# Optimization experiments

Measured on AMD Instinct MI355X. Metric: run time of the kernel, lower is better.

Reference implementation:

```python
import jax, jax.numpy as jnp
import numpy as np

B, S, E, H = 2, 2048, 1024, 16
D = E // H  # head_dim = 64


def _rope(x):
    # x: (B, H, S, D); torchtune-style interleaved rotary embedding
    s, d = x.shape[-2], x.shape[-1]
    inv_freq = 1.0 / (10000.0 ** (jnp.arange(0, d, 2, dtype=jnp.float32) / d))  # (d/2,)
    freqs = jnp.arange(s, dtype=jnp.float32)[:, None] * inv_freq[None, :]       # (S, d/2)
    cos, sin = jnp.cos(freqs), jnp.sin(freqs)
    x1, x2 = x[..., 0::2], x[..., 1::2]
    o1 = x1 * cos - x2 * sin
    o2 = x2 * cos + x1 * sin
    return jnp.stack([o1, o2], axis=-1).reshape(x.shape)


def setup_inputs() -> dict:
    key = jax.random.key(0)
    kx, kq, kk, kv, ko = jax.random.split(key, 5)
    std = 1.0 / np.sqrt(E)
    return {
        "x": jax.random.normal(kx, (B, S, E), dtype=jnp.float32),
        "W_q": jax.random.normal(kq, (E, E), dtype=jnp.float32) * std,
        "W_k": jax.random.normal(kk, (E, E), dtype=jnp.float32) * std,
        "W_v": jax.random.normal(kv, (E, E), dtype=jnp.float32) * std,
        "W_o": jax.random.normal(ko, (E, E), dtype=jnp.float32) * std,
    }


def reference(x, W_q, W_k, W_v, W_o):
    b, s, e = x.shape
    h, d = H, e // H
    # nn.Linear: y = x @ W.T  (weights are (out, in))
    q = (x @ W_q.T).reshape(b, s, h, d).transpose(0, 2, 1, 3)  # (B,H,S,D)
    k = (x @ W_k.T).reshape(b, s, h, d).transpose(0, 2, 1, 3)
    v = (x @ W_v.T).reshape(b, s, h, d).transpose(0, 2, 1, 3)
    q = _rope(q)
    k = _rope(k)
    attn_scale = 1.0 / np.sqrt(e)  # NOTE: scales by sqrt(hidden_dim), as in source
    scores = jnp.einsum("bhsd,bhtd->bhst", q, k) * attn_scale  # (B,H,S,S)
    causal = jnp.triu(jnp.ones((s, s), dtype=bool), k=1)
    scores = jnp.where(causal, -jnp.inf, scores)
    probs = jax.nn.softmax(scores, axis=-1)  # dropout is identity in eval
    out = jnp.einsum("bhst,bhtd->bhsd", probs, v)
    out = out.transpose(0, 2, 1, 3).reshape(b, s, e)
    return out @ W_o.T
```

## Files before the change

### kernel.cpp

```cpp
#include <hip/hip_runtime.h>
#include <hip/hip_bf16.h>

#define BATCH 2
#define SEQ   2048
#define EMB   1024
#define NH    16
#define HD    64
#define MROWS (BATCH*SEQ)
#define NX    (MROWS*EMB)
#define NW    (EMB*EMB)

using f32x4  = __attribute__((ext_vector_type(4))) float;
using bf16x8 = __attribute__((ext_vector_type(8))) short;

#define GLOBAL_AS(p) ((const __attribute__((address_space(1))) void*)(p))
#define LDS_AS(p)    ((__attribute__((address_space(3))) void*)(p))

#define ROPE_L2 0.4152410118609203f
#define QSCALE  0.045084220027780106f

__global__ void fused_cast_kernel(const float* __restrict__ x,
                                  const float* __restrict__ Wq,
                                  const float* __restrict__ Wk,
                                  const float* __restrict__ Wv,
                                  const float* __restrict__ Wo,
                                  __hip_bfloat16* __restrict__ xb,
                                  __hip_bfloat16* __restrict__ Wqkvb,
                                  __hip_bfloat16* __restrict__ Wob) {
    size_t i8 = (size_t)(blockIdx.x * 256 + threadIdx.x) * 8;
    const float* src;
    __hip_bfloat16* dst;
    if (i8 < (size_t)NX) {
        src = x + i8;
        dst = xb + i8;
    } else {
        size_t w = i8 - NX;
        int which = (int)(w >> 20);
        size_t local = w & (NW - 1);
        if (which < 3) {
            src = (which == 0 ? Wq : (which == 1 ? Wk : Wv)) + local;
            dst = Wqkvb + w;
        } else {
            src = Wo + local;
            dst = Wob + local;
        }
    }
    float4 a = *(const float4*)(src);
    float4 b = *(const float4*)(src + 4);
    union { uint4 u; ushort s[8]; } o;
    const float* f = (const float*)&a;
#pragma unroll
    for (int j = 0; j < 4; ++j) {
        __hip_bfloat16 h = __float2bfloat16(f[j]);
        o.s[j] = *(ushort*)&h;
    }
    f = (const float*)&b;
#pragma unroll
    for (int j = 0; j < 4; ++j) {
        __hip_bfloat16 h = __float2bfloat16(f[j]);
        o.s[4 + j] = *(ushort*)&h;
    }
    *(uint4*)dst = o.u;
}

__global__ __launch_bounds__(256) void gemm_qkv_kernel(
        const __hip_bfloat16* __restrict__ A,
        const __hip_bfloat16* __restrict__ W,
        __hip_bfloat16* __restrict__ Qo,
        __hip_bfloat16* __restrict__ Ko,
        __hip_bfloat16* __restrict__ Vo, int M, int K) {
    __shared__ __hip_bfloat16 As[128 * 64];
    __shared__ __hip_bfloat16 Bs[128 * 64];

    const int tid  = threadIdx.x;
    const int wave = tid >> 6;
    const int lane = tid & 63;
    const int quad = lane >> 4;
    const int l16  = lane & 15;
    const int m0   = blockIdx.y * 128;
    const int n0   = blockIdx.x * 128;
    const int wm   = (wave >> 1) * 64;
    const int wn   = (wave & 1) * 64;

    f32x4 acc[4][4] = {};

    for (int k0 = 0; k0 < K; k0 += 64) {
#pragma unroll
        for (int it = 0; it < 4; ++it) {
            int flat = (wave * 4 + it) * 64 + lane;
            int row  = flat >> 3;
            int g    = flat & 7;
            const __hip_bfloat16* ga = A + (size_t)(m0 + row) * K + k0 + g * 8;
            const __hip_bfloat16* gb = W + (size_t)(n0 + row) * K + k0 + g * 8;
            __builtin_amdgcn_global_load_lds(GLOBAL_AS(ga),
                LDS_AS(As + (size_t)(wave * 4 + it) * 512), 16, 0, 0);
            __builtin_amdgcn_global_load_lds(GLOBAL_AS(gb),
                LDS_AS(Bs + (size_t)(wave * 4 + it) * 512), 16, 0, 0);
        }
        __syncthreads();

#pragma unroll
        for (int kk = 0; kk < 2; ++kk) {
            bf16x8 af[4], bfr[4];
#pragma unroll
            for (int i = 0; i < 4; ++i) {
                af[i]  = *(const bf16x8*)(&As[(wm + i * 16 + l16) * 64 + (kk * 4 + quad) * 8]);
                bfr[i] = *(const bf16x8*)(&Bs[(wn + i * 16 + l16) * 64 + (kk * 4 + quad) * 8]);
            }
#pragma unroll
            for (int i = 0; i < 4; ++i)
#pragma unroll
                for (int j = 0; j < 4; ++j)
                    acc[i][j] = __builtin_amdgcn_mfma_f32_16x16x32_bf16(
                        af[i], bfr[j], acc[i][j], 0, 0, 0);
        }
        __syncthreads();
    }

    const int tens = n0 >> 10;
    __hip_bfloat16* outp = (tens == 0) ? Qo : ((tens == 1) ? Ko : Vo);
    const int nbase = n0 & 1023;
#pragma unroll
    for (int i = 0; i < 4; ++i)
#pragma unroll
        for (int j = 0; j < 4; ++j) {
            int col  = nbase + wn + j * 16 + l16;
            int row0 = m0 + wm + i * 16 + quad * 4;
#pragma unroll
            for (int rr = 0; rr < 4; ++rr)
                outp[(size_t)(row0 + rr) * EMB + col] = __float2bfloat16(acc[i][j][rr]);
        }
}

__global__ __launch_bounds__(256) void gemm_oproj_kernel(
        const __hip_bfloat16* __restrict__ A,
        const __hip_bfloat16* __restrict__ Bm,
        float* __restrict__ C, int M, int N, int K) {
    __shared__ __hip_bfloat16 As[128 * 64];
    __shared__ __hip_bfloat16 Bs[64 * 64];

    const int tid  = threadIdx.x;
    const int wave = tid >> 6;
    const int lane = tid & 63;
    const int quad = lane >> 4;
    const int l16  = lane & 15;
    const int m0   = blockIdx.y * 128;
    const int n0   = blockIdx.x * 64;
    const int wm   = (wave >> 1) * 64;
    const int wn   = (wave & 1) * 32;

    f32x4 acc[4][2] = {};

    for (int k0 = 0; k0 < K; k0 += 64) {
#pragma unroll
        for (int it = 0; it < 4; ++it) {
            int flat = (wave * 4 + it) * 64 + lane;
            int row  = flat >> 3;
            int g    = flat & 7;
            const __hip_bfloat16* ga = A + (size_t)(m0 + row) * K + k0 + g * 8;
            __builtin_amdgcn_global_load_lds(GLOBAL_AS(ga),
                LDS_AS(As + (size_t)(wave * 4 + it) * 512), 16, 0, 0);
        }
#pragma unroll
        for (int it = 0; it < 2; ++it) {
            int flat = (wave * 2 + it) * 64 + lane;
            int row  = flat >> 3;
            int g    = flat & 7;
            const __hip_bfloat16* gb = Bm + (size_t)(n0 + row) * K + k0 + g * 8;
            __builtin_amdgcn_global_load_lds(GLOBAL_AS(gb),
                LDS_AS(Bs + (size_t)(wave * 2 + it) * 512), 16, 0, 0);
        }
        __syncthreads();

#pragma unroll
        for (int kk = 0; kk < 2; ++kk) {
            bf16x8 af[4], bfr[2];
#pragma unroll
            for (int i = 0; i < 4; ++i)
                af[i] = *(const bf16x8*)(&As[(wm + i * 16 + l16) * 64 + (kk * 4 + quad) * 8]);
#pragma unroll
            for (int j = 0; j < 2; ++j)
                bfr[j] = *(const bf16x8*)(&Bs[(wn + j * 16 + l16) * 64 + (kk * 4 + quad) * 8]);
#pragma unroll
            for (int i = 0; i < 4; ++i)
#pragma unroll
                for (int j = 0; j < 2; ++j)
                    acc[i][j] = __builtin_amdgcn_mfma_f32_16x16x32_bf16(
                        af[i], bfr[j], acc[i][j], 0, 0, 0);
        }
        __syncthreads();
    }

#pragma unroll
    for (int i = 0; i < 4; ++i)
#pragma unroll
        for (int j = 0; j < 2; ++j) {
            int col  = n0 + wn + j * 16 + l16;
            int row0 = m0 + wm + i * 16 + quad * 4;
#pragma unroll
            for (int rr = 0; rr < 4; ++rr)
                C[(size_t)(row0 + rr) * N + col] = acc[i][j][rr];
        }
}

__global__ void rope_bf16_kernel(__hip_bfloat16* __restrict__ Q,
                                 __hip_bfloat16* __restrict__ K, int n8) {
    int idx = blockIdx.x * blockDim.x + threadIdx.x;
    if (idx >= n8) return;
    int d8 = idx & 7;
    int s  = (idx >> 7) & (SEQ - 1);
    float c[4], sn[4];
#pragma unroll
    for (int j = 0; j < 4; ++j) {
        int i = d8 * 4 + j;
        float inv = exp2f(-(float)i * ROPE_L2);
        float fr  = (float)s * inv;
        c[j]  = cosf(fr);
        sn[j] = sinf(fr);
    }
    size_t base = (size_t)idx * 8;
    uint4 qv = *(uint4*)((char*)Q + base * 2);
    uint4 kv = *(uint4*)((char*)K + base * 2);
    ushort* qe = (ushort*)&qv;
    ushort* ke = (ushort*)&kv;
#pragma unroll
    for (int j = 0; j < 4; ++j) {
        float q1 = __bfloat162float(*(__hip_bfloat16*)&qe[2 * j]);
        float q2 = __bfloat162float(*(__hip_bfloat16*)&qe[2 * j + 1]);
        float o1 = (q1 * c[j] - q2 * sn[j]) * QSCALE;
        float o2 = (q2 * c[j] + q1 * sn[j]) * QSCALE;
        *(__hip_bfloat16*)&qe[2 * j]     = __float2bfloat16(o1);
        *(__hip_bfloat16*)&qe[2 * j + 1] = __float2bfloat16(o2);
        float k1 = __bfloat162float(*(__hip_bfloat16*)&ke[2 * j]);
        float k2 = __bfloat162float(*(__hip_bfloat16*)&ke[2 * j + 1]);
        float p1 = k1 * c[j] - k2 * sn[j];
        float p2 = k2 * c[j] + k1 * sn[j];
        *(__hip_bfloat16*)&ke[2 * j]     = __float2bfloat16(p1);
        *(__hip_bfloat16*)&ke[2 * j + 1] = __float2bfloat16(p2);
    }
    *(uint4*)((char*)Q + base * 2) = qv;
    *(uint4*)((char*)K + base * 2) = kv;
}

__device__ inline uint pack_bf16(float a, float b) {
    __hip_bfloat16 ha = __float2bfloat16(a), hb = __float2bfloat16(b);
    return (uint)*(ushort*)&ha | ((uint)*(ushort*)&hb << 16);
}

__global__ __launch_bounds__(256) void attn_mfma_kernel(
        const __hip_bfloat16* __restrict__ Qb,
        const __hip_bfloat16* __restrict__ Kb,
        const __hip_bfloat16* __restrict__ Vb,
        __hip_bfloat16* __restrict__ Attnb,
        __hip_bfloat16* __restrict__ Opart,
        float* __restrict__ Lpart) {
    const int bx   = blockIdx.x;
    const int bh   = blockIdx.y;
    const int b    = bh >> 4;
    const int h    = bh & (NH - 1);
    const int tid  = threadIdx.x;
    const int wave = tid >> 6;
    const int lane = tid & 63;
    const int quad = lane >> 4;
    const int l16  = lane & 15;

    __shared__ __hip_bfloat16 Ks[2][64 * 64];
    __shared__ uint VTs[2][64][33];

    const int vtp = tid >> 3;
    const int sg  = tid & 7;
    const int lr  = lane >> 3;
    const int lg  = (lane & 7) ^ lr;
    const size_t ksrc_lane = (size_t)lr * EMB + lg * 8;

    const __hip_bfloat16* Kbase = Kb + (size_t)b * SEQ * EMB + h * HD;
    const __hip_bfloat16* Vbase = Vb + (size_t)b * SEQ * EMB + h * HD;

    const bool isA = (bx < 16);
    const int p   = isA ? bx : bx - 16;
    const int q0  = 31 - p;
    const int k00 = isA ? 0 : 17;
    const int n0s = isA ? 17 : (15 - p);
    const int q1  = p;
    const int n1s = isA ? 0 : (p + 1);

    for (int s = 0; s < 2; ++s) {
        const int qt = s ? q1 : q0;
        const int k0 = s ? 0 : k00;
        const int nt = s ? n1s : n0s;
        if (nt <= 0) continue;
        const bool finalSeg = (!isA && s == 1);
        const int wrow = qt * 64 + wave * 16;

        __syncthreads();

        bf16x8 qf[2];
        {
            const __hip_bfloat16* qp =
                Qb + (size_t)(b * SEQ + wrow + l16) * EMB + h * HD + quad * 8;
            qf[0] = *(const bf16x8*)(qp);
            qf[1] = *(const bf16x8*)(qp + 32);
        }

        float lsum = 0.0f;
        f32x4 of[4] = {};

        const __hip_bfloat16* kgp = Kbase + (size_t)k0 * 64 * EMB;
        const __hip_bfloat16* vgp = Vbase + (size_t)(k0 * 64 + 2 * vtp) * EMB + sg * 8;
        uint4 vr0 = *(const uint4*)(vgp);
        uint4 vr1 = *(const uint4*)(vgp + EMB);
#pragma unroll
        for (int it = 0; it < 2; ++it)
            __builtin_amdgcn_global_load_lds(
                GLOBAL_AS(kgp + (size_t)(wave * 2 + it) * 8 * EMB + ksrc_lane),
                LDS_AS(&Ks[0][(wave * 2 + it) * 512]), 16, 0, 0);

        for (int i = 0; i < nt; ++i) {
            const int cur = i & 1;
            const int kt  = k0 + i;

            {
                const ushort* lo = (const ushort*)&vr0;
                const ushort* hi = (const ushort*)&vr1;
#pragma unroll
                for (int e = 0; e < 8; ++e)
                    VTs[cur][sg * 8 + e][vtp] = (uint)lo[e] | ((uint)hi[e] << 16);
            }
            __syncthreads();

            if (i + 1 < nt) {
                kgp += (size_t)64 * EMB;
                vgp += (size_t)64 * EMB;
                vr0 = *(const uint4*)(vgp);
                vr1 = *(const uint4*)(vgp + EMB);
#pragma unroll
                for (int it = 0; it < 2; ++it)
                    __builtin_amdgcn_global_load_lds(
                        GLOBAL_AS(kgp + (size_t)(wave * 2 + it) * 8 * EMB + ksrc_lane),
                        LDS_AS(&Ks[cur ^ 1][(wave * 2 + it) * 512]), 16, 0, 0);
            }

            const bool diag = (kt == qt);
            const __hip_bfloat16* KsC = Ks[cur];
            f32x4 sc[4];
#pragma unroll
            for (int mb = 0; mb < 4; ++mb) {
                f32x4 a = {};
                if (!(diag && mb > wave)) {
                    int krow = mb * 16 + l16;
#pragma unroll
                    for (int kb = 0; kb < 2; ++kb) {
                        int kg = (kb * 4 + quad) ^ (krow & 7);
                        bf16x8 kf = *(const bf16x8*)(&KsC[krow * 64 + kg * 8]);
                        a = __builtin_amdgcn_mfma_f32_16x16x32_bf16(kf, qf[kb], a, 0, 0, 0);
                    }
                }
                sc[mb] = a;
            }

            if (diag) {
#pragma unroll
                for (int mb = 0; mb < 4; ++mb)
#pragma unroll
                    for (int r = 0; r < 4; ++r)
                        if (mb * 16 + quad * 4 + r > wave * 16 + l16)
                            sc[mb][r] = -16384.0f;
            }

#pragma unroll
            for (int mb = 0; mb < 4; ++mb)
#pragma unroll
                for (int r = 0; r < 4; ++r) {
                    float pv = exp2f(sc[mb][r]);
                    sc[mb][r] = pv;
                    lsum += pv;
                }

            bf16x8 pf[2];
            {
                union { uint u[4]; bf16x8 v; } t;
                t.u[0] = pack_bf16(sc[0][0], sc[0][1]);
                t.u[1] = pack_bf16(sc[0][2], sc[0][3]);
                t.u[2] = pack_bf16(sc[1][0], sc[1][1]);
                t.u[3] = pack_bf16(sc[1][2], sc[1][3]);
                pf[0] = t.v;
                t.u[0] = pack_bf16(sc[2][0], sc[2][1]);
                t.u[1] = pack_bf16(sc[2][2], sc[2][3]);
                t.u[2] = pack_bf16(sc[3][0], sc[3][1]);
                t.u[3] = pack_bf16(sc[3][2], sc[3][3]);
                pf[1] = t.v;
            }

            const uint* VT0 = &VTs[cur][0][0];
#pragma unroll
            for (int nb = 0; nb < 4; ++nb) {
                const uint* vrow = VT0 + (size_t)(nb * 16 + l16) * 33;
#pragma unroll
                for (int c = 0; c < 2; ++c) {
                    union { uint u[4]; bf16x8 v; } vf;
                    vf.u[0] = vrow[c * 16 + 2 * quad];
                    vf.u[1] = vrow[c * 16 + 2 * quad + 1];
                    vf.u[2] = vrow[c * 16 + 8 + 2 * quad];
                    vf.u[3] = vrow[c * 16 + 8 + 2 * quad + 1];
                    of[nb] = __builtin_amdgcn_mfma_f32_16x16x32_bf16(
                        pf[c], vf.v, of[nb], 0, 0, 0);
                }
            }
        }

        lsum += __shfl_xor(lsum, 16);
        lsum += __shfl_xor(lsum, 32);
        const int rl0 = quad * 4;
        if (finalSeg) {
            float linv[4];
#pragma unroll
            for (int r = 0; r < 4; ++r)
                linv[r] = 1.0f / __shfl(lsum, rl0 + r);
#pragma unroll
            for (int nb = 0; nb < 4; ++nb)
#pragma unroll
                for (int r = 0; r < 4; ++r) {
                    float v = of[nb][r] * linv[r];
                    Attnb[(size_t)(b * SEQ + wrow + rl0 + r) * EMB + h * HD + nb * 16 + l16] =
                        __float2bfloat16(v);
                }
        } else {
            const int slot = isA ? 0 : 1;
            const size_t lbase = ((size_t)slot * 32 + bh) * SEQ + wrow;
            if (quad == 0)
                Lpart[lbase + l16] = lsum;
#pragma unroll
            for (int nb = 0; nb < 4; ++nb)
#pragma unroll
                for (int r = 0; r < 4; ++r)
                    Opart[(lbase + rl0 + r) * HD + nb * 16 + l16] =
                        __float2bfloat16(of[nb][r]);
        }
    }
}

__global__ void combine_kernel(const __hip_bfloat16* __restrict__ Opart,
                               const float* __restrict__ Lpart,
                               __hip_bfloat16* __restrict__ Attnb) {
    int idx = blockIdx.x * 256 + threadIdx.x;
    int d8 = idx & 7;
    int s  = 1024 + ((idx >> 3) & 1023);
    int bh = idx >> 13;
    int b  = bh >> 4;
    int h  = bh & (NH - 1);
    int qt = s >> 6;

    size_t base0 = ((size_t)bh * SEQ + s) * HD + d8 * 8;
    bf16x8 o0 = *(const bf16x8*)(Opart + base0);
    float l = Lpart[(size_t)bh * SEQ + s];
    float acc[8];
#pragma unroll
    for (int j = 0; j < 8; ++j)
        acc[j] = __uint_as_float(((uint)(ushort)o0[j]) << 16);
    if (qt >= 17) {
        size_t base1 = ((size_t)(32 + bh) * SEQ + s) * HD + d8 * 8;
        bf16x8 o1 = *(const bf16x8*)(Opart + base1);
        l += Lpart[(size_t)(32 + bh) * SEQ + s];
#pragma unroll
        for (int j = 0; j < 8; ++j)
            acc[j] += __uint_as_float(((uint)(ushort)o1[j]) << 16);
    }
    float inv = 1.0f / l;
    union { uint4 u; ushort w[8]; } o;
#pragma unroll
    for (int j = 0; j < 8; ++j) {
        __hip_bfloat16 hv = __float2bfloat16(acc[j] * inv);
        o.w[j] = *(ushort*)&hv;
    }
    *(uint4*)(Attnb + ((size_t)(b * SEQ + s) * EMB) + h * HD + d8 * 8) = o.u;
}

extern "C" void kernel_launch(void* const* d_in, const int* in_sizes, int n_in,
                              void* d_out, int out_size, void* d_ws, size_t ws_size,
                              hipStream_t stream) {
    const float* x  = (const float*)d_in[0];
    const float* Wq = (const float*)d_in[1];
    const float* Wk = (const float*)d_in[2];
    const float* Wv = (const float*)d_in[3];
    const float* Wo = (const float*)d_in[4];
    float* out = (float*)d_out;

    char* ws = (char*)d_ws;
    size_t off = 0;
    auto alloc = [&](size_t bytes) -> void* {
        void* p = ws + off;
        off += (bytes + 255) & ~(size_t)255;
        return p;
    };

    __hip_bfloat16* xb    = (__hip_bfloat16*)alloc((size_t)NX * 2);
    __hip_bfloat16* Wqkvb = (__hip_bfloat16*)alloc((size_t)NW * 3 * 2);
    __hip_bfloat16* Wob   = (__hip_bfloat16*)alloc((size_t)NW * 2);
    __hip_bfloat16* Qbuf  = (__hip_bfloat16*)alloc((size_t)NX * 2);
    __hip_bfloat16* Kbuf  = (__hip_bfloat16*)alloc((size_t)NX * 2);
    __hip_bfloat16* Vbuf  = (__hip_bfloat16*)alloc((size_t)NX * 2);
    __hip_bfloat16* Attnb = (__hip_bfloat16*)alloc((size_t)NX * 2);
    __hip_bfloat16* Opart = (__hip_bfloat16*)alloc((size_t)2 * 32 * SEQ * HD * 2);
    float*          Lpart = (float*)alloc((size_t)2 * 32 * SEQ * 4);

    fused_cast_kernel<<<(NX + 4 * NW) / (256 * 8), 256, 0, stream>>>(
        x, Wq, Wk, Wv, Wo, xb, Wqkvb, Wob);

    dim3 qgrid(24, MROWS / 128);
    gemm_qkv_kernel<<<qgrid, 256, 0, stream>>>(xb, Wqkvb, Qbuf, Kbuf, Vbuf,
                                               MROWS, EMB);

    const int n8 = NX / 8;
    rope_bf16_kernel<<<n8 / 256, 256, 0, stream>>>(Qbuf, Kbuf, n8);

    dim3 agrid(32, BATCH * NH);
    attn_mfma_kernel<<<agrid, 256, 0, stream>>>(Qbuf, Kbuf, Vbuf, Attnb,
                                                Opart, Lpart);

    combine_kernel<<<(32 * 1024 * 8) / 256, 256, 0, stream>>>(Opart, Lpart, Attnb);

    dim3 ggrid(EMB / 64, MROWS / 128);
    gemm_oproj_kernel<<<ggrid, 256, 0, stream>>>(Attnb, Wob, out, MROWS, EMB, EMB);
}
```

Measured before the change: 206.3 us.

## Fuse RoPE into QKV GEMM epilogue and XOR-swizzle GEMM LDS tiles

```diff
diff --git a/kernel.cpp b/kernel.cpp
--- a/kernel.cpp
+++ b/kernel.cpp
@@ -26,7 +26,20 @@
                                   const float* __restrict__ Wo,
                                   __hip_bfloat16* __restrict__ xb,
                                   __hip_bfloat16* __restrict__ Wqkvb,
-                                  __hip_bfloat16* __restrict__ Wob) {
+                                  __hip_bfloat16* __restrict__ Wob,
+                                  float2* __restrict__ ctab) {
+    if (blockIdx.x >= 4096) {
+        int e  = (blockIdx.x - 4096) * 256 + threadIdx.x;
+        int s  = e >> 5;
+        int ip = e & 31;
+        float inv = exp2f(-(float)ip * ROPE_L2);
+        float fr  = (float)s * inv;
+        float2 cs;
+        cs.x = cosf(fr);
+        cs.y = sinf(fr);
+        ctab[e] = cs;
+        return;
+    }
     size_t i8 = (size_t)(blockIdx.x * 256 + threadIdx.x) * 8;
     const float* src;
     __hip_bfloat16* dst;
@@ -68,7 +81,8 @@
         const __hip_bfloat16* __restrict__ W,
         __hip_bfloat16* __restrict__ Qo,
         __hip_bfloat16* __restrict__ Ko,
-        __hip_bfloat16* __restrict__ Vo, int M, int K) {
+        __hip_bfloat16* __restrict__ Vo,
+        const float2* __restrict__ ctab, int M, int K) {
     __shared__ __hip_bfloat16 As[128 * 64];
     __shared__ __hip_bfloat16 Bs[128 * 64];
 
@@ -81,6 +95,7 @@
     const int n0   = blockIdx.x * 128;
     const int wm   = (wave >> 1) * 64;
     const int wn   = (wave & 1) * 64;
+    const int xr   = l16 & 7;
 
     f32x4 acc[4][4] = {};
 
@@ -89,7 +104,7 @@
         for (int it = 0; it < 4; ++it) {
             int flat = (wave * 4 + it) * 64 + lane;
             int row  = flat >> 3;
-            int g    = flat & 7;
+            int g    = (flat & 7) ^ (row & 7);
             const __hip_bfloat16* ga = A + (size_t)(m0 + row) * K + k0 + g * 8;
             const __hip_bfloat16* gb = W + (size_t)(n0 + row) * K + k0 + g * 8;
             __builtin_amdgcn_global_load_lds(GLOBAL_AS(ga),
@@ -101,11 +116,12 @@
 
 #pragma unroll
         for (int kk = 0; kk < 2; ++kk) {
+            const int kg = (kk * 4 + quad) ^ xr;
             bf16x8 af[4], bfr[4];
 #pragma unroll
             for (int i = 0; i < 4; ++i) {
-                af[i]  = *(const bf16x8*)(&As[(wm + i * 16 + l16) * 64 + (kk * 4 + quad) * 8]);
-                bfr[i] = *(const bf16x8*)(&Bs[(wn + i * 16 + l16) * 64 + (kk * 4 + quad) * 8]);
+                af[i]  = *(const bf16x8*)(&As[(wm + i * 16 + l16) * 64 + kg * 8]);
+                bfr[i] = *(const bf16x8*)(&Bs[(wn + i * 16 + l16) * 64 + kg * 8]);
             }
 #pragma unroll
             for (int i = 0; i < 4; ++i)
@@ -120,16 +136,38 @@
     const int tens = n0 >> 10;
     __hip_bfloat16* outp = (tens == 0) ? Qo : ((tens == 1) ? Ko : Vo);
     const int nbase = n0 & 1023;
-#pragma unroll
-    for (int i = 0; i < 4; ++i)
-#pragma unroll
-        for (int j = 0; j < 4; ++j) {
-            int col  = nbase + wn + j * 16 + l16;
-            int row0 = m0 + wm + i * 16 + quad * 4;
-#pragma unroll
-            for (int rr = 0; rr < 4; ++rr)
-                outp[(size_t)(row0 + rr) * EMB + col] = __float2bfloat16(acc[i][j][rr]);
-        }
+    if (tens < 2) {
+        const float sgn   = (l16 & 1) ? 1.0f : -1.0f;
+        const float qmul  = (tens == 0) ? QSCALE : 1.0f;
+#pragma unroll
+        for (int i = 0; i < 4; ++i)
+#pragma unroll
+            for (int j = 0; j < 4; ++j) {
+                int col  = nbase + wn + j * 16 + l16;
+                int ip   = ((wn + j * 16 + l16) & 63) >> 1;
+                int row0 = m0 + wm + i * 16 + quad * 4;
+#pragma unroll
+                for (int rr = 0; rr < 4; ++rr) {
+                    float v = acc[i][j][rr];
+                    float p = __shfl_xor(v, 1);
+                    int sp  = (row0 + rr) & (SEQ - 1);
+                    float2 cs = ctab[sp * 32 + ip];
+                    float o = (v * cs.x + sgn * p * cs.y) * qmul;
+                    outp[(size_t)(row0 + rr) * EMB + col] = __float2bfloat16(o);
+                }
+            }
+    } else {
+#pragma unroll
+        for (int i = 0; i < 4; ++i)
+#pragma unroll
+            for (int j = 0; j < 4; ++j) {
+                int col  = nbase + wn + j * 16 + l16;
+                int row0 = m0 + wm + i * 16 + quad * 4;
+#pragma unroll
+                for (int rr = 0; rr < 4; ++rr)
+                    outp[(size_t)(row0 + rr) * EMB + col] = __float2bfloat16(acc[i][j][rr]);
+            }
+    }
 }
 
 __global__ __launch_bounds__(256) void gemm_oproj_kernel(
@@ -148,6 +186,7 @@
     const int n0   = blockIdx.x * 64;
     const int wm   = (wave >> 1) * 64;
     const int wn   = (wave & 1) * 32;
+    const int xr   = l16 & 7;
 
     f32x4 acc[4][2] = {};
 
@@ -156,7 +195,7 @@
         for (int it = 0; it < 4; ++it) {
             int flat = (wave * 4 + it) * 64 + lane;
             int row  = flat >> 3;
-            int g    = flat & 7;
+            int g    = (flat & 7) ^ (row & 7);
             const __hip_bfloat16* ga = A + (size_t)(m0 + row) * K + k0 + g * 8;
             __builtin_amdgcn_global_load_lds(GLOBAL_AS(ga),
                 LDS_AS(As + (size_t)(wave * 4 + it) * 512), 16, 0, 0);
@@ -165,7 +204,7 @@
         for (int it = 0; it < 2; ++it) {
             int flat = (wave * 2 + it) * 64 + lane;
             int row  = flat >> 3;
-            int g    = flat & 7;
+            int g    = (flat & 7) ^ (row & 7);
             const __hip_bfloat16* gb = Bm + (size_t)(n0 + row) * K + k0 + g * 8;
             __builtin_amdgcn_global_load_lds(GLOBAL_AS(gb),
                 LDS_AS(Bs + (size_t)(wave * 2 + it) * 512), 16, 0, 0);
@@ -174,13 +213,14 @@
 
 #pragma unroll
         for (int kk = 0; kk < 2; ++kk) {
+            const int kg = (kk * 4 + quad) ^ xr;
             bf16x8 af[4], bfr[2];
 #pragma unroll
             for (int i = 0; i < 4; ++i)
-                af[i] = *(const bf16x8*)(&As[(wm + i * 16 + l16) * 64 + (kk * 4 + quad) * 8]);
+                af[i] = *(const bf16x8*)(&As[(wm + i * 16 + l16) * 64 + kg * 8]);
 #pragma unroll
             for (int j = 0; j < 2; ++j)
-                bfr[j] = *(const bf16x8*)(&Bs[(wn + j * 16 + l16) * 64 + (kk * 4 + quad) * 8]);
+                bfr[j] = *(const bf16x8*)(&Bs[(wn + j * 16 + l16) * 64 + kg * 8]);
 #pragma unroll
             for (int i = 0; i < 4; ++i)
 #pragma unroll
@@ -201,45 +241,6 @@
             for (int rr = 0; rr < 4; ++rr)
                 C[(size_t)(row0 + rr) * N + col] = acc[i][j][rr];
         }
-}
-
-__global__ void rope_bf16_kernel(__hip_bfloat16* __restrict__ Q,
-                                 __hip_bfloat16* __restrict__ K, int n8) {
-    int idx = blockIdx.x * blockDim.x + threadIdx.x;
-    if (idx >= n8) return;
-    int d8 = idx & 7;
-    int s  = (idx >> 7) & (SEQ - 1);
-    float c[4], sn[4];
-#pragma unroll
-    for (int j = 0; j < 4; ++j) {
-        int i = d8 * 4 + j;
-        float inv = exp2f(-(float)i * ROPE_L2);
-        float fr  = (float)s * inv;
-        c[j]  = cosf(fr);
-        sn[j] = sinf(fr);
-    }
-    size_t base = (size_t)idx * 8;
-    uint4 qv = *(uint4*)((char*)Q + base * 2);
-    uint4 kv = *(uint4*)((char*)K + base * 2);
-    ushort* qe = (ushort*)&qv;
-    ushort* ke = (ushort*)&kv;
-#pragma unroll
-    for (int j = 0; j < 4; ++j) {
-        float q1 = __bfloat162float(*(__hip_bfloat16*)&qe[2 * j]);
-        float q2 = __bfloat162float(*(__hip_bfloat16*)&qe[2 * j + 1]);
-        float o1 = (q1 * c[j] - q2 * sn[j]) * QSCALE;
-        float o2 = (q2 * c[j] + q1 * sn[j]) * QSCALE;
-        *(__hip_bfloat16*)&qe[2 * j]     = __float2bfloat16(o1);
-        *(__hip_bfloat16*)&qe[2 * j + 1] = __float2bfloat16(o2);
-        float k1 = __bfloat162float(*(__hip_bfloat16*)&ke[2 * j]);
-        float k2 = __bfloat162float(*(__hip_bfloat16*)&ke[2 * j + 1]);
-        float p1 = k1 * c[j] - k2 * sn[j];
-        float p2 = k2 * c[j] + k1 * sn[j];
-        *(__hip_bfloat16*)&ke[2 * j]     = __float2bfloat16(p1);
-        *(__hip_bfloat16*)&ke[2 * j + 1] = __float2bfloat16(p2);
-    }
-    *(uint4*)((char*)Q + base * 2) = qv;
-    *(uint4*)((char*)K + base * 2) = kv;
 }
 
 __device__ inline uint pack_bf16(float a, float b) {
@@ -502,16 +503,14 @@
     __hip_bfloat16* Attnb = (__hip_bfloat16*)alloc((size_t)NX * 2);
     __hip_bfloat16* Opart = (__hip_bfloat16*)alloc((size_t)2 * 32 * SEQ * HD * 2);
     float*          Lpart = (float*)alloc((size_t)2 * 32 * SEQ * 4);
-
-    fused_cast_kernel<<<(NX + 4 * NW) / (256 * 8), 256, 0, stream>>>(
-        x, Wq, Wk, Wv, Wo, xb, Wqkvb, Wob);
+    float2*         ctab  = (float2*)alloc((size_t)SEQ * 32 * sizeof(float2));
+
+    fused_cast_kernel<<<(NX + 4 * NW) / (256 * 8) + 256, 256, 0, stream>>>(
+        x, Wq, Wk, Wv, Wo, xb, Wqkvb, Wob, ctab);
 
     dim3 qgrid(24, MROWS / 128);
     gemm_qkv_kernel<<<qgrid, 256, 0, stream>>>(xb, Wqkvb, Qbuf, Kbuf, Vbuf,
-                                               MROWS, EMB);
-
-    const int n8 = NX / 8;
-    rope_bf16_kernel<<<n8 / 256, 256, 0, stream>>>(Qbuf, Kbuf, n8);
+                                               ctab, MROWS, EMB);
 
     dim3 agrid(32, BATCH * NH);
     attn_mfma_kernel<<<agrid, 256, 0, stream>>>(Qbuf, Kbuf, Vbuf, Attnb,
```

Measured after the change: 196.1 us. -5.0%, faster.
